# Performance work log

Measured on AMD Instinct MI355X. Metric: run time of the kernel, lower is better.

Reference implementation:

```python
import jax, jax.numpy as jnp
import numpy as np

NINP = 512
NHEAD = 8


def setup_inputs() -> dict:
    key = jax.random.key(0)
    ks = jax.random.split(key, 7)
    B, M, L, C = 2, 32, 512, NINP
    s = 1.0 / np.sqrt(C)
    return {
        "x": jax.random.normal(ks[0], (B, M, L, C), dtype=jnp.float32),
        "Wq": jax.random.normal(ks[1], (C, C), dtype=jnp.float32) * s,
        "bq": jax.random.normal(ks[2], (C,), dtype=jnp.float32) * s,
        "Wk": jax.random.normal(ks[3], (C, C), dtype=jnp.float32) * s,
        "bk": jax.random.normal(ks[4], (C,), dtype=jnp.float32) * s,
        "Wv": jax.random.normal(ks[5], (C, C), dtype=jnp.float32) * s,
        "bv": jax.random.normal(ks[6], (C,), dtype=jnp.float32) * s,
    }


def reference(x, Wq, bq, Wk, bk, Wv, bv) -> jnp.ndarray:
    # x: (B, M, L, C). Attention over L within each (B, M) block.
    B, M, L, C = x.shape
    H = NHEAD
    D = C // H
    scale = 1.0 / jnp.sqrt(jnp.asarray(D, dtype=x.dtype))

    def split_heads(t):  # (B,M,L,C) -> (B,M,H,L,D)
        return t.reshape(B, M, L, H, D).transpose(0, 1, 3, 2, 4)

    q = split_heads(x @ Wq + bq)
    k = split_heads(x @ Wk + bk)
    v = split_heads(x @ Wv + bv)

    scores = jnp.einsum("bmhid,bmhjd->bmhij", q, k) * scale
    w = jax.nn.softmax(scores, axis=-1)  # dropout p=0 -> identity
    out = jnp.einsum("bmhij,bmhjd->bmhid", w, v)  # (B,M,H,L,D)
    return out.transpose(0, 1, 3, 2, 4).reshape(B, M, L, C)
```

## Files before the change

kernel.cpp:

```cpp
#include <hip/hip_runtime.h>


typedef unsigned short u16;
typedef unsigned int u32;
typedef unsigned long long u64;
typedef __bf16 bf16x8 __attribute__((ext_vector_type(8)));
typedef float f32x4 __attribute__((ext_vector_type(4)));

#define SCQ 0.18033688011112042f

static __device__ __forceinline__ u16 f2bf(float f) {
  u32 x = __float_as_uint(f);
  x += 0x7fffu + ((x >> 16) & 1u);
  return (u16)(x >> 16);
}

static __device__ __forceinline__ u32 pkbf(float f0, float f1) {
  return __builtin_amdgcn_perm(__float_as_uint(f1) + 0x8000u,
                               __float_as_uint(f0) + 0x8000u, 0x07060302u);
}

typedef __attribute__((address_space(1))) const void* gvp;
typedef __attribute__((address_space(3))) void* lvp;
static __device__ __forceinline__ void glds16(const void* g, void* l) {
  __builtin_amdgcn_global_load_lds((gvp)g, (lvp)l, 16, 0, 0);
}

__global__ __launch_bounds__(256) void prep(const float* __restrict__ x,
                                            u16* __restrict__ xb,
                                            const float* __restrict__ Wq,
                                            const float* __restrict__ Wk,
                                            const float* __restrict__ Wv,
                                            u16* __restrict__ WT) {
  __shared__ float t[32][33];
  const int bx = blockIdx.x;
  if (bx < 8192) {
    const u32 i = (bx * 256u + threadIdx.x) * 8u;
    const float4 a = *(const float4*)(x + i);
    const float4 b = *(const float4*)(x + i + 4);
    union { u16 r[8]; uint4 v; } u;
    u.r[0] = f2bf(a.x); u.r[1] = f2bf(a.y); u.r[2] = f2bf(a.z); u.r[3] = f2bf(a.w);
    u.r[4] = f2bf(b.x); u.r[5] = f2bf(b.y); u.r[6] = f2bf(b.z); u.r[7] = f2bf(b.w);
    *(uint4*)(xb + i) = u.v;
    return;
  }
  const int b = bx - 8192;
  const int z = b >> 8;
  const int rem = b & 255;
  const float* W = (z == 0) ? Wq : ((z == 1) ? Wk : Wv);
  u16* dst = WT + z * 262144;
  const int k0 = (rem >> 4) * 32, n0 = (rem & 15) * 32;
  const int tx = threadIdx.x & 31, ty = threadIdx.x >> 5;
#pragma unroll
  for (int i = 0; i < 32; i += 8)
    t[ty + i][tx] = W[(size_t)(k0 + ty + i) * 512 + n0 + tx];
  __syncthreads();
#pragma unroll
  for (int i = 0; i < 32; i += 8)
    dst[(size_t)(n0 + ty + i) * 512 + k0 + tx] = f2bf(t[tx][ty + i]);
}

__global__ __launch_bounds__(256) void gemm_qkv(const u16* __restrict__ xb,
                                                const u16* __restrict__ WT,
                                                const float* __restrict__ bq,
                                                const float* __restrict__ bk,
                                                const float* __restrict__ bv,
                                                u16* __restrict__ qkv) {
  __shared__ __align__(16) u16 smem[8192];
  u16* sA = smem;
  u16* sB = smem + 4096;
  const int z = blockIdx.z;
  const u16* Bg = WT + z * 262144;
  const float* bias = (z == 0) ? bq : ((z == 1) ? bk : bv);
  u16* out = qkv + (size_t)z * 16777216u;
  const int tid = threadIdx.x;
  const int lane = tid & 63;
  const int w = tid >> 6;
  const int wy = w >> 1, wx = w & 1;
  const int m15 = lane & 15, g = lane >> 4;
  const int mbase = blockIdx.x * 128;
  const int nbase = blockIdx.y * 128;

  const int srow = w * 32 + (lane >> 2);
  const int scol = (lane & 3) * 8;
  const u16* Ap = xb + (size_t)(mbase + srow) * 512 + scol;
  const u16* Bp = Bg + (size_t)(nbase + srow) * 512 + scol;
  u16* sAw = sA + w * 1024;
  u16* sBw = sB + w * 1024;

  f32x4 acc[4][4] = {};

  for (int kt = 0; kt < 16; ++kt) {
    const int k0 = kt * 32;
    glds16(Ap + k0, sAw);
    glds16(Ap + k0 + 16 * 512, sAw + 512);
    glds16(Bp + k0, sBw);
    glds16(Bp + k0 + 16 * 512, sBw + 512);
    __syncthreads();
    bf16x8 af[4], bfr[4];
#pragma unroll
    for (int t = 0; t < 4; ++t)
      af[t] = *(const bf16x8*)&sA[(wy * 64 + t * 16 + m15) * 32 + g * 8];
#pragma unroll
    for (int t = 0; t < 4; ++t)
      bfr[t] = *(const bf16x8*)&sB[(wx * 64 + t * 16 + m15) * 32 + g * 8];
#pragma unroll
    for (int rt = 0; rt < 4; ++rt)
#pragma unroll
      for (int ct = 0; ct < 4; ++ct)
        acc[rt][ct] =
            __builtin_amdgcn_mfma_f32_16x16x32_bf16(af[rt], bfr[ct], acc[rt][ct], 0, 0, 0);
    __syncthreads();
  }

  if (z < 2) {
    const float sc = (z == 0) ? SCQ : 1.0f;
#pragma unroll
    for (int ct = 0; ct < 4; ++ct) {
      const int col = nbase + wx * 64 + ct * 16 + m15;
      const float bb = bias[col];
#pragma unroll
      for (int rt = 0; rt < 4; ++rt) {
        const int row0 = mbase + wy * 64 + rt * 16 + g * 4;
#pragma unroll
        for (int r = 0; r < 4; ++r)
          out[(size_t)(row0 + r) * 512 + col] = f2bf((acc[rt][ct][r] + bb) * sc);
      }
    }
  } else {
    const int bm = mbase >> 9, jb = mbase & 511;
    u16* sT = smem;
#pragma unroll
    for (int cn = 0; cn < 4; ++cn) {
      __syncthreads();
      if (wx == (cn >> 1)) {
#pragma unroll
        for (int cte = 0; cte < 2; ++cte) {
          const int ct = (cn & 1) * 2 + cte;
          const int ncol = nbase + wx * 64 + ct * 16 + m15;
          const float bb = bias[ncol];
          const int nl = cte * 16 + m15;
#pragma unroll
          for (int rt = 0; rt < 4; ++rt) {
            u64 pk = 0;
#pragma unroll
            for (int r = 0; r < 4; ++r)
              pk |= (u64)f2bf(acc[rt][ct][r] + bb) << (16 * r);
            *(u64*)&sT[nl * 136 + wy * 64 + rt * 16 + g * 4] = pk;
          }
        }
      }
      __syncthreads();
#pragma unroll
      for (int it = 0; it < 2; ++it) {
        const int nl = it * 16 + (tid >> 4);
        const int ml = (tid & 15) * 8;
        const int ng = nbase + cn * 32 + nl;
        const int h = ng >> 6, d = ng & 63;
        *(uint4*)(out + ((size_t)((bm * 8 + h) * 64 + d)) * 512 + jb + ml) =
            *(const uint4*)&sT[nl * 136 + ml];
      }
    }
  }
}

__global__ __launch_bounds__(256) void attn(const u16* __restrict__ Q,
                                            const u16* __restrict__ K,
                                            const u16* __restrict__ Vt,
                                            float* __restrict__ out) {
  __shared__ __align__(16) char smem[36864];
  u16* sK = (u16*)smem;
  u16* sVT = (u16*)(smem + 9216);
  const int tid = threadIdx.x;
  const int lane = tid & 63;
  const int w = tid >> 6;
  const int m15 = lane & 15, g = lane >> 4;
  const int qt = blockIdx.x, h = blockIdx.y, bm = blockIdx.z;
  const size_t rb = (size_t)bm * 512;
  const int q0 = qt * 128 + w * 32;
  u16* sPT = (u16*)(smem + 18432) + w * 2304;

  bf16x8 qf[2][2];
#pragma unroll
  for (int ct = 0; ct < 2; ++ct)
#pragma unroll
    for (int kc = 0; kc < 2; ++kc)
      qf[ct][kc] =
          *(const bf16x8*)(Q + (rb + q0 + ct * 16 + m15) * 512 + h * 64 + kc * 32 + g * 8);

  f32x4 acc[4][2] = {};
  f32x4 lv[2] = {};

  const int srow = tid >> 3, sc8 = (tid & 7) * 8;
  const u16* Kb = K + rb * 512 + h * 64;
  const u16* Vtb = Vt + (size_t)(bm * 8 + h) * 64 * 512;

  for (int jt = 0; jt < 8; ++jt) {
    const int j0 = jt * 64;
    const uint4 k0v = *(const uint4*)(Kb + (size_t)(j0 + srow) * 512 + sc8);
    const uint4 k1v = *(const uint4*)(Kb + (size_t)(j0 + srow + 32) * 512 + sc8);
    const uint4 v0v = *(const uint4*)(Vtb + (size_t)srow * 512 + j0 + sc8);
    const uint4 v1v = *(const uint4*)(Vtb + (size_t)(srow + 32) * 512 + j0 + sc8);
    __syncthreads();
    *(uint4*)&sK[srow * 72 + sc8] = k0v;
    *(uint4*)&sK[(srow + 32) * 72 + sc8] = k1v;
    *(uint4*)&sVT[srow * 72 + sc8] = v0v;
    *(uint4*)&sVT[(srow + 32) * 72 + sc8] = v1v;
    __syncthreads();

    f32x4 s[4][2];
#pragma unroll
    for (int rt = 0; rt < 4; ++rt) {
      const bf16x8 k0 = *(const bf16x8*)&sK[(rt * 16 + m15) * 72 + g * 8];
      const bf16x8 k1 = *(const bf16x8*)&sK[(rt * 16 + m15) * 72 + 32 + g * 8];
#pragma unroll
      for (int ct = 0; ct < 2; ++ct) {
        f32x4 z = {};
        z = __builtin_amdgcn_mfma_f32_16x16x32_bf16(k0, qf[ct][0], z, 0, 0, 0);
        s[rt][ct] = __builtin_amdgcn_mfma_f32_16x16x32_bf16(k1, qf[ct][1], z, 0, 0, 0);
      }
    }

#pragma unroll
    for (int ct = 0; ct < 2; ++ct)
#pragma unroll
      for (int rt = 0; rt < 4; ++rt) {
        f32x4 p;
#pragma unroll
        for (int r = 0; r < 4; ++r) p[r] = exp2f(s[rt][ct][r]);
        lv[ct] += p;
        uint2 pk = {pkbf(p[0], p[1]), pkbf(p[2], p[3])};
        *(uint2*)&sPT[(ct * 16 + m15) * 72 + rt * 16 + g * 4] = pk;
      }

    bf16x8 pb[2][2];
#pragma unroll
    for (int ct = 0; ct < 2; ++ct)
#pragma unroll
      for (int kc = 0; kc < 2; ++kc)
        pb[ct][kc] = *(const bf16x8*)&sPT[(ct * 16 + m15) * 72 + kc * 32 + g * 8];
#pragma unroll
    for (int dt = 0; dt < 4; ++dt) {
      const bf16x8 v0 = *(const bf16x8*)&sVT[(dt * 16 + m15) * 72 + g * 8];
      const bf16x8 v1 = *(const bf16x8*)&sVT[(dt * 16 + m15) * 72 + 32 + g * 8];
#pragma unroll
      for (int ct = 0; ct < 2; ++ct) {
        acc[dt][ct] = __builtin_amdgcn_mfma_f32_16x16x32_bf16(v0, pb[ct][0], acc[dt][ct], 0, 0, 0);
        acc[dt][ct] = __builtin_amdgcn_mfma_f32_16x16x32_bf16(v1, pb[ct][1], acc[dt][ct], 0, 0, 0);
      }
    }
  }

  float inv[2];
#pragma unroll
  for (int ct = 0; ct < 2; ++ct) {
    float l = lv[ct][0] + lv[ct][1] + lv[ct][2] + lv[ct][3];
    l += __shfl_xor(l, 16);
    l += __shfl_xor(l, 32);
    inv[ct] = 1.0f / l;
  }
  __syncthreads();
  float* sO = (float*)(smem + w * 4608);
#pragma unroll
  for (int c = 0; c < 2; ++c) {
#pragma unroll
    for (int dt2 = 0; dt2 < 2; ++dt2)
#pragma unroll
      for (int ct = 0; ct < 2; ++ct) {
        f32x4 v = acc[c * 2 + dt2][ct] * inv[ct];
        *(f32x4*)&sO[(ct * 16 + m15) * 36 + dt2 * 16 + g * 4] = v;
      }
#pragma unroll
    for (int it = 0; it < 4; ++it) {
      const int q = it * 8 + (lane >> 3);
      f32x4 v = *(const f32x4*)&sO[q * 36 + (lane & 7) * 4];
      *(f32x4*)&out[(rb + q0 + q) * 512 + h * 64 + c * 32 + (lane & 7) * 4] = v;
    }
  }
}

extern "C" void kernel_launch(void* const* d_in, const int* in_sizes, int n_in,
                              void* d_out, int out_size, void* d_ws, size_t ws_size,
                              hipStream_t stream) {
  const float* x = (const float*)d_in[0];
  const float* Wq = (const float*)d_in[1];
  const float* bq = (const float*)d_in[2];
  const float* Wk = (const float*)d_in[3];
  const float* bk = (const float*)d_in[4];
  const float* Wv = (const float*)d_in[5];
  const float* bv = (const float*)d_in[6];
  float* out = (float*)d_out;

  u16* ws = (u16*)d_ws;
  u16* xb = ws;
  u16* WT = ws + 16777216;
  u16* qkv = ws + 17563648;

  prep<<<8960, 256, 0, stream>>>(x, xb, Wq, Wk, Wv, WT);
  gemm_qkv<<<dim3(256, 4, 3), 256, 0, stream>>>(xb, WT, bq, bk, bv, qkv);
  attn<<<dim3(4, 8, 64), 256, 0, stream>>>(qkv, qkv + 16777216, qkv + 2 * 16777216, out);
}
```

Before: 281.0 us.

## Double-buffer LDS in QKV GEMM and prefetch K/V tiles in attention

The QKV projection GEMM now uses two LDS buffers, so the async global-to-LDS load of the next K slice overlaps the MFMA work on the current one. The attention kernel prefetches the next K/V tile into registers while the current tile is processed, with explicit waitcnt and barrier placement. The aim is to hide global memory latency behind compute, at the cost of double the GEMM LDS footprint (possibly lower occupancy) and more live registers.

```diff
diff --git a/kernel.cpp b/kernel.cpp
--- a/kernel.cpp
+++ b/kernel.cpp
@@ -66,9 +66,7 @@
                                                 const float* __restrict__ bk,
                                                 const float* __restrict__ bv,
                                                 u16* __restrict__ qkv) {
-  __shared__ __align__(16) u16 smem[8192];
-  u16* sA = smem;
-  u16* sB = smem + 4096;
+  __shared__ __align__(16) u16 smem[16384];
   const int z = blockIdx.z;
   const u16* Bg = WT + z * 262144;
   const float* bias = (z == 0) ? bq : ((z == 1) ? bk : bv);
@@ -85,33 +83,52 @@
   const int scol = (lane & 3) * 8;
   const u16* Ap = xb + (size_t)(mbase + srow) * 512 + scol;
   const u16* Bp = Bg + (size_t)(nbase + srow) * 512 + scol;
-  u16* sAw = sA + w * 1024;
-  u16* sBw = sB + w * 1024;
+
+  u16* buf0 = smem;
+  u16* buf1 = smem + 8192;
 
   f32x4 acc[4][4] = {};
 
-  for (int kt = 0; kt < 16; ++kt) {
-    const int k0 = kt * 32;
-    glds16(Ap + k0, sAw);
-    glds16(Ap + k0 + 16 * 512, sAw + 512);
-    glds16(Bp + k0, sBw);
-    glds16(Bp + k0 + 16 * 512, sBw + 512);
-    __syncthreads();
-    bf16x8 af[4], bfr[4];
-#pragma unroll
-    for (int t = 0; t < 4; ++t)
-      af[t] = *(const bf16x8*)&sA[(wy * 64 + t * 16 + m15) * 32 + g * 8];
-#pragma unroll
-    for (int t = 0; t < 4; ++t)
-      bfr[t] = *(const bf16x8*)&sB[(wx * 64 + t * 16 + m15) * 32 + g * 8];
-#pragma unroll
-    for (int rt = 0; rt < 4; ++rt)
-#pragma unroll
-      for (int ct = 0; ct < 4; ++ct)
-        acc[rt][ct] =
-            __builtin_amdgcn_mfma_f32_16x16x32_bf16(af[rt], bfr[ct], acc[rt][ct], 0, 0, 0);
-    __syncthreads();
-  }
+#define STAGE(KT, B)                                  \
+  do {                                                \
+    const int k0_ = (KT) * 32;                        \
+    u16* d_ = (B) + w * 1024;                         \
+    glds16(Ap + k0_, d_);                             \
+    glds16(Ap + k0_ + 16 * 512, d_ + 512);            \
+    glds16(Bp + k0_, d_ + 4096);                      \
+    glds16(Bp + k0_ + 16 * 512, d_ + 4096 + 512);     \
+  } while (0)
+
+#define COMPUTE(B)                                                          \
+  do {                                                                      \
+    bf16x8 af[4], bfr[4];                                                   \
+    _Pragma("unroll") for (int t = 0; t < 4; ++t)                           \
+        af[t] = *(const bf16x8*)&(B)[(wy * 64 + t * 16 + m15) * 32 + g * 8];\
+    _Pragma("unroll") for (int t = 0; t < 4; ++t)                           \
+        bfr[t] = *(const bf16x8*)&(B)[4096 + (wx * 64 + t * 16 + m15) * 32 + g * 8]; \
+    _Pragma("unroll") for (int rt = 0; rt < 4; ++rt)                        \
+        _Pragma("unroll") for (int ct = 0; ct < 4; ++ct)                    \
+            acc[rt][ct] = __builtin_amdgcn_mfma_f32_16x16x32_bf16(          \
+                af[rt], bfr[ct], acc[rt][ct], 0, 0, 0);                     \
+  } while (0)
+
+  STAGE(0, buf0);
+  asm volatile("s_waitcnt vmcnt(0)" ::: "memory");
+  __builtin_amdgcn_s_barrier();
+
+#pragma unroll
+  for (int kt = 0; kt < 16; kt += 2) {
+    if (kt + 1 < 16) STAGE(kt + 1, buf1);
+    COMPUTE(buf0);
+    asm volatile("s_waitcnt vmcnt(0) lgkmcnt(0)" ::: "memory");
+    __builtin_amdgcn_s_barrier();
+    if (kt + 2 < 16) STAGE(kt + 2, buf0);
+    COMPUTE(buf1);
+    asm volatile("s_waitcnt vmcnt(0) lgkmcnt(0)" ::: "memory");
+    __builtin_amdgcn_s_barrier();
+  }
+#undef STAGE
+#undef COMPUTE
 
   if (z < 2) {
     const float sc = (z == 0) ? SCQ : 1.0f;
@@ -195,18 +212,28 @@
   const u16* Kb = K + rb * 512 + h * 64;
   const u16* Vtb = Vt + (size_t)(bm * 8 + h) * 64 * 512;
 
+  uint4 k0v = *(const uint4*)(Kb + (size_t)srow * 512 + sc8);
+  uint4 k1v = *(const uint4*)(Kb + (size_t)(srow + 32) * 512 + sc8);
+  uint4 v0v = *(const uint4*)(Vtb + (size_t)srow * 512 + sc8);
+  uint4 v1v = *(const uint4*)(Vtb + (size_t)(srow + 32) * 512 + sc8);
+
   for (int jt = 0; jt < 8; ++jt) {
-    const int j0 = jt * 64;
-    const uint4 k0v = *(const uint4*)(Kb + (size_t)(j0 + srow) * 512 + sc8);
-    const uint4 k1v = *(const uint4*)(Kb + (size_t)(j0 + srow + 32) * 512 + sc8);
-    const uint4 v0v = *(const uint4*)(Vtb + (size_t)srow * 512 + j0 + sc8);
-    const uint4 v1v = *(const uint4*)(Vtb + (size_t)(srow + 32) * 512 + j0 + sc8);
-    __syncthreads();
+    asm volatile("s_waitcnt lgkmcnt(0)" ::: "memory");
+    __builtin_amdgcn_s_barrier();
+    asm volatile("s_waitcnt vmcnt(0)" ::: "memory");
     *(uint4*)&sK[srow * 72 + sc8] = k0v;
     *(uint4*)&sK[(srow + 32) * 72 + sc8] = k1v;
     *(uint4*)&sVT[srow * 72 + sc8] = v0v;
     *(uint4*)&sVT[(srow + 32) * 72 + sc8] = v1v;
-    __syncthreads();
+    if (jt < 7) {
+      const int j1 = (jt + 1) * 64;
+      k0v = *(const uint4*)(Kb + (size_t)(j1 + srow) * 512 + sc8);
+      k1v = *(const uint4*)(Kb + (size_t)(j1 + srow + 32) * 512 + sc8);
+      v0v = *(const uint4*)(Vtb + (size_t)srow * 512 + j1 + sc8);
+      v1v = *(const uint4*)(Vtb + (size_t)(srow + 32) * 512 + j1 + sc8);
+    }
+    asm volatile("s_waitcnt lgkmcnt(0)" ::: "memory");
+    __builtin_amdgcn_s_barrier();
 
     f32x4 s[4][2];
 #pragma unroll
```

Result: faster. 270.7 us (-3.7%).
